# Performance work log

Measured on AMD Instinct MI355X. Metric: run time of the kernel, lower is better.

The kernel has to match this reference:

```python
import jax, jax.numpy as jnp
import numpy as np

F_, V, ED = 16, 1000, 16
B = 65536
D_IN = F_ * ED            # 256
STAR = [256, 512, 256]    # star layers
FCN = [256, 128, 64]      # mmoe expert layers
DOM, TSK, EXP = 3, 2, 8
KDT = DOM * TSK           # 6 gates/towers
SKIP_WEIGHT = 0.5
EPS = 1e-5


def layernorm(x, g, b):
    mu = jnp.mean(x, -1, keepdims=True)
    var = jnp.mean((x - mu) ** 2, -1, keepdims=True)
    return (x - mu) * jax.lax.rsqrt(var + EPS) * g + b


def mlp1(x, W, b, g, be):
    # Linear -> LayerNorm -> ReLU (MLP_N with one block)
    return jax.nn.relu(layernorm(x @ W + b, g, be))


def stack2(h, W1, b1, g1, be1, W2, b2, g2, be2):
    # vectorized bank of 2-block MLP_N experts; h: [B,D0], W1: [E,D0,D1]
    h1 = jax.nn.relu(layernorm(jnp.einsum('bd,edh->ebh', h, W1) + b1[:, None, :], g1[:, None, :], be1[:, None, :]))
    h2 = jax.nn.relu(layernorm(jnp.einsum('ebd,edh->ebh', h1, W2) + b2[:, None, :], g2[:, None, :], be2[:, None, :]))
    return h2  # [E,B,H]


def setup_inputs() -> dict:
    key = jax.random.key(0)
    ks = iter(jax.random.split(key, 64))

    def nrm(shape, scale=0.05):
        return jax.random.normal(next(ks), shape, jnp.float32) * scale

    inp = {}
    inp['x'] = jax.random.randint(next(ks), (F_, B), 0, 3).astype(jnp.int32)
    inp['emb_tables'] = nrm((F_, V, ED))
    inp['skip_W'] = nrm((D_IN, STAR[2])); inp['skip_b'] = jnp.zeros((STAR[2],))
    inp['skip_g'] = jnp.ones((STAR[2],)); inp['skip_be'] = jnp.zeros((STAR[2],))
    inp['shared_W'] = nrm((STAR[0], STAR[1])); inp['shared_b'] = jnp.zeros((STAR[1],))
    inp['slot_W'] = nrm((DOM, STAR[0], STAR[1])); inp['slot_b'] = jnp.zeros((DOM, STAR[1]))
    inp['star_W'] = nrm((STAR[1], STAR[2])); inp['star_b'] = jnp.zeros((STAR[2],))
    inp['star_g'] = jnp.ones((STAR[2],)); inp['star_be'] = jnp.zeros((STAR[2],))
    inp['dskip_W'] = nrm((KDT, STAR[2], FCN[-1])); inp['dskip_b'] = jnp.zeros((KDT, FCN[-1]))
    inp['dskip_g'] = jnp.ones((KDT, FCN[-1])); inp['dskip_be'] = jnp.zeros((KDT, FCN[-1]))
    for pre, n in (('exp', EXP), ('dexp', DOM), ('texp', TSK)):
        inp[pre + '_W1'] = nrm((n, FCN[0], FCN[1])); inp[pre + '_b1'] = jnp.zeros((n, FCN[1]))
        inp[pre + '_g1'] = jnp.ones((n, FCN[1])); inp[pre + '_be1'] = jnp.zeros((n, FCN[1]))
        inp[pre + '_W2'] = nrm((n, FCN[1], FCN[2])); inp[pre + '_b2'] = jnp.zeros((n, FCN[2]))
        inp[pre + '_g2'] = jnp.ones((n, FCN[2])); inp[pre + '_be2'] = jnp.zeros((n, FCN[2]))
    inp['gate_W'] = nrm((KDT, FCN[0], EXP)); inp['gate_b'] = jnp.zeros((KDT, EXP))
    inp['tow_W1'] = nrm((KDT, FCN[-1], FCN[-1])); inp['tow_b1'] = jnp.zeros((KDT, FCN[-1]))
    inp['tow_g'] = jnp.ones((KDT, FCN[-1])); inp['tow_be'] = jnp.zeros((KDT, FCN[-1]))
    inp['tow_W2'] = nrm((KDT, FCN[-1])); inp['tow_b2'] = jnp.zeros((KDT,))
    return inp


def _forward(x, emb_tables, skip_W, skip_b, skip_g, skip_be, shared_W, shared_b,
             slot_W, slot_b, star_W, star_b, star_g, star_be,
             dskip_W, dskip_b, dskip_g, dskip_be,
             exp_W1, exp_b1, exp_g1, exp_be1, exp_W2, exp_b2, exp_g2, exp_be2,
             dexp_W1, dexp_b1, dexp_g1, dexp_be1, dexp_W2, dexp_b2, dexp_g2, dexp_be2,
             texp_W1, texp_b1, texp_g1, texp_be1, texp_W2, texp_b2, texp_g2, texp_be2,
             gate_W, gate_b, tow_W1, tow_b1, tow_g, tow_be, tow_W2, tow_b2):
    domain_id = x[-1]                                          # [B] in {0,1,2}
    embs = jax.vmap(lambda t, i: t[i])(emb_tables, x)          # [F,B,ED]
    input_emb = jnp.moveaxis(embs, 0, 1).reshape(x.shape[1], D_IN)  # [B,256]

    skip = mlp1(input_emb, skip_W, skip_b, skip_g, skip_be)    # [B,256]

    # STAR: per-domain elementwise-product weights, domain masked select
    slot_out = jnp.einsum('bd,kdh->kbh', input_emb, slot_W * shared_W[None]) + slot_b[:, None, :] + shared_b  # [D,B,512]
    onehot = (domain_id[None, :] == jnp.arange(DOM)[:, None]).astype(slot_out.dtype)  # [D,B]
    emb0 = jnp.sum(onehot[:, :, None] * slot_out, axis=0)      # [B,512]
    emb = mlp1(emb0, star_W, star_b, star_g, star_be) + skip   # [B,256]

    # gates use emb.detach()
    gate = jax.nn.softmax(jnp.einsum('bd,kde->kbe', jax.lax.stop_gradient(emb), gate_W) + gate_b[:, None, :], axis=-1)  # [6,B,8]

    fea = stack2(emb, exp_W1, exp_b1, exp_g1, exp_be1, exp_W2, exp_b2, exp_g2, exp_be2)        # [8,B,64]
    dfea = stack2(emb, dexp_W1, dexp_b1, dexp_g1, dexp_be1, dexp_W2, dexp_b2, dexp_g2, dexp_be2)  # [3,B,64]
    tfea = stack2(emb, texp_W1, texp_b1, texp_g1, texp_be1, texp_W2, texp_b2, texp_g2, texp_be2)  # [2,B,64]
    dskip = jax.nn.relu(layernorm(jnp.einsum('bd,kdh->kbh', emb, dskip_W) + dskip_b[:, None, :], dskip_g[:, None, :], dskip_be[:, None, :]))  # [6,B,64]

    d_idx = jnp.arange(KDT) % DOM
    t_idx = jnp.arange(KDT) % TSK
    fused = jnp.einsum('kbe,ebh->kbh', gate, fea) + dfea[d_idx] + tfea[t_idx] + SKIP_WEIGHT * dskip  # [6,B,64]

    h = jax.nn.relu(layernorm(jnp.einsum('kbh,khj->kbj', fused, tow_W1) + tow_b1[:, None, :], tow_g[:, None, :], tow_be[:, None, :]))
    probs = jax.nn.sigmoid(jnp.einsum('kbh,kh->kb', h, tow_W2) + tow_b2[:, None])  # [6,B]

    # output[:, i] with i = t*DOM + d -> [B,T,D]; pick per-sample domain column
    out = jnp.moveaxis(probs, 0, 1).reshape(-1, TSK, DOM)
    result = jnp.take_along_axis(out, domain_id[:, None, None].astype(jnp.int32), axis=2)[:, :, 0]  # [B,T]
    return result


def reference(x, emb_tables, skip_W, skip_b, skip_g, skip_be, shared_W, shared_b,
              slot_W, slot_b, star_W, star_b, star_g, star_be,
              dskip_W, dskip_b, dskip_g, dskip_be,
              exp_W1, exp_b1, exp_g1, exp_be1, exp_W2, exp_b2, exp_g2, exp_be2,
              dexp_W1, dexp_b1, dexp_g1, dexp_be1, dexp_W2, dexp_b2, dexp_g2, dexp_be2,
              texp_W1, texp_b1, texp_g1, texp_be1, texp_W2, texp_b2, texp_g2, texp_be2,
              gate_W, gate_b, tow_W1, tow_b1, tow_g, tow_be, tow_W2, tow_b2):
    return _forward(x, emb_tables, skip_W, skip_b, skip_g, skip_be, shared_W, shared_b,
                    slot_W, slot_b, star_W, star_b, star_g, star_be,
                    dskip_W, dskip_b, dskip_g, dskip_be,
                    exp_W1, exp_b1, exp_g1, exp_be1, exp_W2, exp_b2, exp_g2, exp_be2,
                    dexp_W1, dexp_b1, dexp_g1, dexp_be1, dexp_W2, dexp_b2, dexp_g2, dexp_be2,
                    texp_W1, texp_b1, texp_g1, texp_be1, texp_W2, texp_b2, texp_g2, texp_be2,
                    gate_W, gate_b, tow_W1, tow_b1, tow_g, tow_be, tow_W2, tow_b2)
```

## Files before the change

### kernel.cpp

```cpp
#include <hip/hip_runtime.h>
#include <stdint.h>

#define B_TOT 65536

typedef __attribute__((ext_vector_type(8))) short s16x8;
typedef __attribute__((ext_vector_type(4))) float f32x4;
typedef unsigned short u16;
typedef unsigned int u32;

#define OFF_SKIPW   0
#define OFF_MD      65536
#define OFF_GATEW   262144
#define OFF_EXPW1   274432
#define OFF_EXPW2   700416
#define OFF_DSKIPW  806912
#define OFF_TOWW1   905216
#define OFF_BVEC    929792
#define OFF_PAR     931328
#define OFF_PARF    941568
#define OFF_EMB     944640

#define PAR_DSK  7488
#define PAR_TOW  8640
#define PAR_GB   10176
#define PAR_TB2  10224

__device__ __forceinline__ float bf2f(u16 h){ u32 v=((u32)h)<<16; return __builtin_bit_cast(float,v); }
__device__ __forceinline__ u16 f2bf(float f){
  u32 u=__builtin_bit_cast(u32,f);
  u += 0x7fffu + ((u>>16)&1u);
  return (u16)(u>>16);
}
__device__ __forceinline__ f32x4 mfma16(s16x8 a, s16x8 b, f32x4 c){
  return __builtin_amdgcn_mfma_f32_16x16x32_bf16(a,b,c,0,0,0);
}
__device__ __forceinline__ void lds_fence(){ asm volatile("s_waitcnt lgkmcnt(0)" ::: "memory"); }

__device__ __forceinline__ void gstage(const u16* gsrc, u16* ldsdst, int nbytes, int wv, int lane, int nw){
  for(int off = wv*1024; off < nbytes; off += nw*1024){
    __builtin_amdgcn_global_load_lds(
      (const __attribute__((address_space(1))) u32*)((const char*)gsrc + off + lane*16),
      (__attribute__((address_space(3))) u32*)((char*)ldsdst + off),
      16, 0, 0);
  }
}

template<int NT>
__device__ __forceinline__ void ln16(const f32x4* a, float invN, float* mu, float* rs){
  float s[4], q[4];
#pragma unroll
  for(int r=0;r<4;r++){ float aa=0.f,bb=0.f;
#pragma unroll
    for(int t=0;t<NT;t++){ float v=a[t][r]; aa+=v; bb+=v*v; }
    s[r]=aa; q[r]=bb; }
#pragma unroll
  for(int m=1;m<16;m<<=1){
#pragma unroll
    for(int r=0;r<4;r++){ s[r]+=__shfl_xor(s[r],m,16); q[r]+=__shfl_xor(q[r],m,16); } }
#pragma unroll
  for(int r=0;r<4;r++){ float m_=s[r]*invN; float v=q[r]*invN-m_*m_; mu[r]=m_; rs[r]=rsqrtf(v+1e-5f); }
}

__global__ __launch_bounds__(256) void k_pack(
    const float* __restrict__ skip_W, const float* __restrict__ gate_W,
    const float* __restrict__ exp_W1, const float* __restrict__ dexp_W1, const float* __restrict__ texp_W1,
    const float* __restrict__ exp_W2, const float* __restrict__ dexp_W2, const float* __restrict__ texp_W2,
    const float* __restrict__ dskip_W, const float* __restrict__ tow_W1,
    u16* __restrict__ ws)
{
  int i=blockIdx.x*256+threadIdx.x;
  if(i>=OFF_BVEC) return;
  if(i>=OFF_MD && i<OFF_GATEW) return;
  float v;
  if(i<OFF_MD){
    int l=i; int j=l&7, lane=(l>>3)&63, kt=(l>>9)&7, ct=l>>12;
    int n=ct*16+(lane&15), k=kt*32+((lane>>4)<<3)+j;
    v = skip_W[k*256+n];
  } else if(i<OFF_EXPW1){
    int l=i-OFF_GATEW; int j=l&7, lane=(l>>3)&63, kt=(l>>9)&7, ct=l>>12;
    int n=ct*16+(lane&15), k=kt*32+((lane>>4)<<3)+j;
    int k6=n>>3, e=n&7;
    v = gate_W[(k6*256+k)*8+e];
  } else if(i<OFF_EXPW2){
    int l=i-OFF_EXPW1; int e=l>>15, r=l&32767;
    int j=r&7, lane=(r>>3)&63, kt=(r>>9)&7, ct=r>>12;
    int n=ct*16+(lane&15), k=kt*32+((lane>>4)<<3)+j;
    v = (e<8)? exp_W1[(e*256+k)*128+n] : (e<11)? dexp_W1[((e-8)*256+k)*128+n] : texp_W1[((e-11)*256+k)*128+n];
  } else if(i<OFF_DSKIPW){
    int l=i-OFF_EXPW2; int e=l>>13, r=l&8191;
    int j=r&7, lane=(r>>3)&63, kt=(r>>9)&3, ct=r>>11;
    int n=ct*16+(lane&15), k=kt*32+((lane>>4)<<3)+j;
    v = (e<8)? exp_W2[(e*128+k)*64+n] : (e<11)? dexp_W2[((e-8)*128+k)*64+n] : texp_W2[((e-11)*128+k)*64+n];
  } else if(i<OFF_TOWW1){
    int l=i-OFF_DSKIPW; int s=l>>14, r=l&16383;
    int j=r&7, lane=(r>>3)&63, kt=(r>>9)&7, ct=r>>12;
    int n=ct*16+(lane&15), k=kt*32+((lane>>4)<<3)+j;
    v = dskip_W[(s*256+k)*64+n];
  } else {
    int l=i-OFF_TOWW1; int s=l>>12, r=l&4095;
    int j=r&7, lane=(r>>3)&63, kt=(r>>9)&1, ct=r>>10;
    int n=ct*16+(lane&15), k=kt*32+((lane>>4)<<3)+j;
    v = tow_W1[(s*64+k)*64+n];
  }
  ws[i]=f2bf(v);
}

__global__ __launch_bounds__(256) void k_packpar(
    const float* __restrict__ exp_b1,const float* __restrict__ exp_g1,const float* __restrict__ exp_be1,
    const float* __restrict__ exp_b2,const float* __restrict__ exp_g2,const float* __restrict__ exp_be2,
    const float* __restrict__ dexp_b1,const float* __restrict__ dexp_g1,const float* __restrict__ dexp_be1,
    const float* __restrict__ dexp_b2,const float* __restrict__ dexp_g2,const float* __restrict__ dexp_be2,
    const float* __restrict__ texp_b1,const float* __restrict__ texp_g1,const float* __restrict__ texp_be1,
    const float* __restrict__ texp_b2,const float* __restrict__ texp_g2,const float* __restrict__ texp_be2,
    const float* __restrict__ dskip_b,const float* __restrict__ dskip_g,const float* __restrict__ dskip_be,
    const float* __restrict__ gate_b,
    const float* __restrict__ tow_b1,const float* __restrict__ tow_g,const float* __restrict__ tow_be,
    const float* __restrict__ tow_W2,const float* __restrict__ tow_b2,
    const float* __restrict__ skip_b,const float* __restrict__ skip_g,const float* __restrict__ skip_be,
    const float* __restrict__ star_b,const float* __restrict__ star_g,const float* __restrict__ star_be,
    u16* __restrict__ ws)
{
  int i=blockIdx.x*256+threadIdx.x;
  float* parf=(float*)(ws+OFF_PARF);
  if(i<10240){
    float v=0.f;
    if(i<PAR_DSK){
      int e=i/576, r=i%576;
      const float *b1,*g1,*be1,*b2,*g2,*be2;
      if(e<8){ b1=exp_b1+e*128; g1=exp_g1+e*128; be1=exp_be1+e*128;
               b2=exp_b2+e*64;  g2=exp_g2+e*64;  be2=exp_be2+e*64; }
      else if(e<11){ int q=e-8; b1=dexp_b1+q*128; g1=dexp_g1+q*128; be1=dexp_be1+q*128;
               b2=dexp_b2+q*64; g2=dexp_g2+q*64; be2=dexp_be2+q*64; }
      else { int q=e-11; b1=texp_b1+q*128; g1=texp_g1+q*128; be1=texp_be1+q*128;
               b2=texp_b2+q*64; g2=texp_g2+q*64; be2=texp_be2+q*64; }
      v = (r<128)? b1[r] : (r<256)? g1[r-128] : (r<384)? be1[r-256]
        : (r<448)? b2[r-384] : (r<512)? g2[r-448] : be2[r-512];
    } else if(i<PAR_TOW){
      int l=i-PAR_DSK; int j=l/192, r=l%192;
      v = (r<64)? dskip_b[j*64+r] : (r<128)? dskip_g[j*64+r-64] : dskip_be[j*64+r-128];
    } else if(i<PAR_GB){
      int l=i-PAR_TOW; int k6=l/256, r=l%256;
      v = (r<64)? tow_b1[k6*64+r] : (r<128)? tow_g[k6*64+r-64]
        : (r<192)? tow_be[k6*64+r-128] : tow_W2[k6*64+r-192];
    } else if(i<PAR_TB2){ v=gate_b[i-PAR_GB]; }
    else if(i<PAR_TB2+6){ v=tow_b2[i-PAR_TB2]; }
    ws[OFF_PAR+i]=f2bf(v);
  } else if(i<10240+1536){
    int l=i-10240;
    parf[l] = (l<256)? skip_b[l] : (l<512)? skip_g[l-256] : (l<768)? skip_be[l-512]
            : (l<1024)? star_b[l-768] : (l<1280)? star_g[l-1024] : star_be[l-1280];
  }
}

__global__ __launch_bounds__(256) void k_fold(
    const float* __restrict__ slot_W, const float* __restrict__ shared_W, const float* __restrict__ star_W,
    const float* __restrict__ slot_b, const float* __restrict__ shared_b,
    u16* __restrict__ ws)
{
  __shared__ float w[512];
  int bid=blockIdx.x, tid=threadIdx.x;
  if(bid<768){
    int d=bid>>8, k=bid&255;
    for(int j=tid;j<512;j+=256) w[j]=slot_W[(d*256+k)*512+j]*shared_W[k*512+j];
    __syncthreads();
    int n=tid; float a=0.f;
    for(int j=0;j<512;j++) a += w[j]*star_W[j*256+n];
    int ct=n>>4, l15=n&15, kt=k>>5, hi=(k>>3)&3, j8=k&7;
    ws[OFF_MD + d*65536 + (((ct*8+kt)*64 + hi*16 + l15)<<3) + j8] = f2bf(a);
  } else {
    int d=bid-768;
    for(int j=tid;j<512;j+=256) w[j]=slot_b[d*512+j]+shared_b[j];
    __syncthreads();
    int n=tid; float a=0.f;
    for(int j=0;j<512;j++) a += w[j]*star_W[j*256+n];
    ((float*)(ws+OFF_BVEC))[d*256+n]=a;
  }
}

__global__ __launch_bounds__(256,2) void k_front(
    const int* __restrict__ x, const float* __restrict__ emb_tables,
    u16* __restrict__ wsu)
{
  __shared__ __align__(16) u16 shbuf[33792];
  __shared__ float bvecL[768];
  __shared__ float parF[1536];

  const int tid=threadIdx.x, lane=tid&63, wv=tid>>6;
  const int l15=lane&15, hq=lane>>4;
  const int b0=blockIdx.x*128, rowbase=b0+wv*32;
  const f32x4 fz={0.f,0.f,0.f,0.f};
  const s16x8 zf={0,0,0,0,0,0,0,0};
  u16* Wb[2]={shbuf, shbuf+8192};
  u16* trbw = shbuf + wv*8448;
  u16* embp = wsu+OFF_EMB;

  gstage(wsu+OFF_SKIPW, Wb[0], 16384, wv, lane, 4);
  gstage(wsu+OFF_BVEC, (u16*)bvecL, 3072, wv, lane, 4);
  gstage(wsu+OFF_PARF, (u16*)parF, 6144, wv, lane, 4);

  int dmA[2], dm[2][4];
#pragma unroll
  for(int rt=0;rt<2;rt++){
    dmA[rt]=x[15*B_TOT + rowbase + rt*16 + l15];
#pragma unroll
    for(int r=0;r<4;r++) dm[rt][r]=x[15*B_TOT + rowbase + rt*16 + hq*4 + r];
  }

  s16x8 af[2][8];
#pragma unroll
  for(int rt=0;rt<2;rt++){
#pragma unroll
    for(int kt=0;kt<8;kt++){
      int f=kt*2+(hq>>1), j0=(hq&1)*8;
      int row=rowbase+rt*16+l15;
      int idx=x[f*B_TOT+row];
      const float* sp=emb_tables + (size_t)(f*1000+idx)*16 + j0;
      float4 v0=*(const float4*)sp, v1=*(const float4*)(sp+4);
      union{ u16 h[8]; s16x8 v; } t;
      t.h[0]=f2bf(v0.x); t.h[1]=f2bf(v0.y); t.h[2]=f2bf(v0.z); t.h[3]=f2bf(v0.w);
      t.h[4]=f2bf(v1.x); t.h[5]=f2bf(v1.y); t.h[6]=f2bf(v1.z); t.h[7]=f2bf(v1.w);
      af[rt][kt]=t.v;
    }
  }
  __syncthreads();
  int cur=0;

  f32x4 acc[2][16];
#pragma unroll
  for(int rt=0;rt<2;rt++)
#pragma unroll
    for(int ct=0;ct<16;ct++) acc[rt][ct]=fz;

#pragma unroll
  for(int c=0;c<8;c++){
    if(c<7) gstage(wsu+OFF_SKIPW+(c+1)*8192, Wb[cur^1], 16384, wv, lane, 4);
    const u16* B=Wb[cur];
#pragma unroll
    for(int kt=0;kt<8;kt++){
#pragma unroll
      for(int i=0;i<2;i++){
        s16x8 bf=*(const s16x8*)(B + (((i*8+kt)*64+lane)<<3));
        acc[0][c*2+i]=mfma16(af[0][kt],bf,acc[0][c*2+i]);
        acc[1][c*2+i]=mfma16(af[1][kt],bf,acc[1][c*2+i]);
      }
    }
    __syncthreads(); cur^=1;
  }
#pragma unroll
  for(int rt=0;rt<2;rt++){
#pragma unroll
    for(int ct=0;ct<16;ct++){ float bb=parF[ct*16+l15];
#pragma unroll
      for(int r=0;r<4;r++) acc[rt][ct][r]+=bb; }
    float mu[4],rs[4];
    ln16<16>(&acc[rt][0], 1.f/256.f, mu, rs);
#pragma unroll
    for(int ct=0;ct<16;ct++){
      int col=ct*16+l15;
      float gv=parF[256+col], bev=parF[512+col];
#pragma unroll
      for(int r=0;r<4;r++){
        float v=fmaxf((acc[rt][ct][r]-mu[r])*rs[r]*gv+bev,0.f);
        trbw[(rt*16+hq*4+r)*264 + col]=f2bf(v);
      }
    }
  }
  lds_fence();
#pragma unroll
  for(int rt=0;rt<2;rt++){
    int rtg=(b0>>4)+wv*2+rt;
#pragma unroll
    for(int kt=0;kt<8;kt++){
      s16x8 v=*(const s16x8*)(trbw + (rt*16+l15)*264 + kt*32+hq*8);
      *(s16x8*)(embp + (((size_t)(rtg*8+kt)*64+lane)<<3)) = v;
    }
  }
  __syncthreads();
  gstage(wsu+OFF_MD, Wb[0], 16384, wv, lane, 4);
  __syncthreads();
  cur=0;

#pragma unroll
  for(int rt=0;rt<2;rt++)
#pragma unroll
    for(int ct=0;ct<16;ct++) acc[rt][ct]=fz;
  for(int d=0;d<3;d++){
#pragma unroll
    for(int c=0;c<8;c++){
      if(c<7)      gstage(wsu+OFF_MD+d*65536+(c+1)*8192, Wb[cur^1], 16384, wv, lane, 4);
      else if(d<2) gstage(wsu+OFF_MD+(d+1)*65536,        Wb[cur^1], 16384, wv, lane, 4);
      const u16* B=Wb[cur];
#pragma unroll
      for(int kt=0;kt<8;kt++){
        s16x8 a0=(dmA[0]==d)?af[0][kt]:zf;
        s16x8 a1=(dmA[1]==d)?af[1][kt]:zf;
#pragma unroll
        for(int i=0;i<2;i++){
          s16x8 bf=*(const s16x8*)(B + (((i*8+kt)*64+lane)<<3));
          acc[0][c*2+i]=mfma16(a0,bf,acc[0][c*2+i]);
          acc[1][c*2+i]=mfma16(a1,bf,acc[1][c*2+i]);
        }
      }
      __syncthreads(); cur^=1;
    }
  }

#pragma unroll
  for(int rt=0;rt<2;rt++){
#pragma unroll
    for(int ct=0;ct<16;ct++){
      int col=ct*16+l15; float sb=parF[768+col];
#pragma unroll
      for(int r=0;r<4;r++) acc[rt][ct][r] += sb + bvecL[dm[rt][r]*256+col];
    }
    float mu[4],rs[4];
    ln16<16>(&acc[rt][0], 1.f/256.f, mu, rs);
#pragma unroll
    for(int ct=0;ct<16;ct++){
      int col=ct*16+l15;
      float gv=parF[1024+col], bev=parF[1280+col];
#pragma unroll
      for(int r=0;r<4;r++){
        float v=fmaxf((acc[rt][ct][r]-mu[r])*rs[r]*gv+bev,0.f);
        trbw[(rt*16+hq*4+r)*264 + col]=f2bf(v);
      }
    }
  }
  lds_fence();
#pragma unroll
  for(int rt=0;rt<2;rt++){
    int rtg=(b0>>4)+wv*2+rt;
#pragma unroll
    for(int kt=0;kt<8;kt++){
      s16x8 vs=*(const s16x8*)(trbw + (rt*16+l15)*264 + kt*32+hq*8);
      s16x8 vk=*(const s16x8*)(embp + (((size_t)(rtg*8+kt)*64+lane)<<3));
      union{ u16 h[8]; s16x8 v; } t;
#pragma unroll
      for(int j=0;j<8;j++) t.h[j]=f2bf(bf2f((u16)vs[j])+bf2f((u16)vk[j]));
      *(s16x8*)(embp + (((size_t)(rtg*8+kt)*64+lane)<<3)) = t.v;
    }
  }
}

__device__ __forceinline__ int phase_off(int p){
  if(p<2)  return OFF_GATEW + p*8192;
  if(p<67){ int q=p-2, u=q/5, s=q%5;
            return (s<4)? (OFF_EXPW1+u*32768+s*8192) : (OFF_EXPW2+u*8192); }
  if(p<79){ int q=p-67; return OFF_DSKIPW + (q>>1)*16384 + (q&1)*8192; }
  return OFF_TOWW1 + (p-79)*8192;
}
__device__ __forceinline__ void stage16k(const u16* g, u16* l, int wv, int lane){
  __builtin_amdgcn_global_load_lds(
    (const __attribute__((address_space(1))) u32*)((const char*)g + wv*1024 + lane*16),
    (__attribute__((address_space(3))) u32*)((char*)l + wv*1024), 16,0,0);
  __builtin_amdgcn_global_load_lds(
    (const __attribute__((address_space(1))) u32*)((const char*)g + 8192 + wv*1024 + lane*16),
    (__attribute__((address_space(3))) u32*)((char*)l + 8192 + wv*1024), 16,0,0);
}
__device__ __forceinline__ void endph2(){ asm volatile("s_waitcnt vmcnt(2)\n\ts_barrier" ::: "memory"); }
__device__ __forceinline__ void endph0(){ asm volatile("s_waitcnt vmcnt(0)\n\ts_barrier" ::: "memory"); }

__global__ __launch_bounds__(512,2) void k_B(
    const int* __restrict__ x, u16* __restrict__ wsu, float* __restrict__ out)
{
  __shared__ __align__(16) u16 Wb[3][8192];
  __shared__ __align__(16) u16 trb[8][32][136];
  __shared__ __align__(16) u16 parAll[10240];
  __shared__ __align__(16) u32 gateF[256][8];

  const int tid=threadIdx.x, lane=tid&63, wv=tid>>6;
  const int l15=lane&15, hq=lane>>4;
  const int b0=blockIdx.x*256, rowbase=b0+wv*32;
  const f32x4 fz={0.f,0.f,0.f,0.f};
  const u16* embp=wsu+OFF_EMB;
  u16* trbw=&trb[wv][0][0];

  gstage(wsu+OFF_PAR, parAll, 20480, wv, lane, 8);
  stage16k(wsu+phase_off(0), &Wb[0][0], wv, lane);
  stage16k(wsu+phase_off(1), &Wb[1][0], wv, lane);

  int dm[2][4];
#pragma unroll
  for(int rt=0;rt<2;rt++)
#pragma unroll
    for(int r=0;r<4;r++) dm[rt][r]=x[15*B_TOT + rowbase + rt*16 + hq*4 + r];

  s16x8 af[2][8];
#pragma unroll
  for(int rt=0;rt<2;rt++){
    int rtg=(rowbase>>4)+rt;
#pragma unroll
    for(int kt=0;kt<8;kt++)
      af[rt][kt]=*(const s16x8*)(embp + (((size_t)(rtg*8+kt)*64+lane)<<3));
  }

  f32x4 fa0[2][4], fa1[2][4];
#pragma unroll
  for(int rt=0;rt<2;rt++)
#pragma unroll
    for(int ct=0;ct<4;ct++){ fa0[rt][ct]=fz; fa1[rt][ct]=fz; }

  __syncthreads();
  int p=0;

  {
    f32x4 gacc[2][3];
#pragma unroll
    for(int rt=0;rt<2;rt++)
#pragma unroll
      for(int ct=0;ct<3;ct++) gacc[rt][ct]=fz;
    stage16k(wsu+phase_off(2), &Wb[2][0], wv, lane);
#pragma unroll
    for(int kt=0;kt<8;kt++)
#pragma unroll
      for(int i=0;i<2;i++){
        s16x8 bf=*(const s16x8*)(&Wb[0][0] + (((i*8+kt)*64+lane)<<3));
        gacc[0][i]=mfma16(af[0][kt],bf,gacc[0][i]);
        gacc[1][i]=mfma16(af[1][kt],bf,gacc[1][i]);
      }
    endph2(); p=1;

    stage16k(wsu+phase_off(3), &Wb[0][0], wv, lane);
#pragma unroll
    for(int kt=0;kt<8;kt++){
      s16x8 bf=*(const s16x8*)(&Wb[1][0] + ((kt*64+lane)<<3));
      gacc[0][2]=mfma16(af[0][kt],bf,gacc[0][2]);
      gacc[1][2]=mfma16(af[1][kt],bf,gacc[1][2]);
    }
    u16* gFh=(u16*)&gateF[0][0];
#pragma unroll
    for(int rt=0;rt<2;rt++)
#pragma unroll
      for(int ct=0;ct<3;ct++){
        int k6=ct*2+(l15>>3), e=l15&7;
        float gb=bf2f(parAll[PAR_GB + k6*8+e]);
#pragma unroll
        for(int r=0;r<4;r++){
          float v=gacc[rt][ct][r]+gb;
          float mx=v;
          mx=fmaxf(mx,__shfl_xor(mx,1,8)); mx=fmaxf(mx,__shfl_xor(mx,2,8)); mx=fmaxf(mx,__shfl_xor(mx,4,8));
          float pe=__expf(v-mx);
          float ss=pe;
          ss+=__shfl_xor(ss,1,8); ss+=__shfl_xor(ss,2,8); ss+=__shfl_xor(ss,4,8);
          int brow=wv*32+rt*16+hq*4+r;
          int dmv=dm[rt][r];
          if(k6==dmv)   gFh[(brow*8+e)*2]  =f2bf(pe/ss);
          if(k6==3+dmv) gFh[(brow*8+e)*2+1]=f2bf(pe/ss);
        }
      }
    lds_fence();
    endph2(); p=2;
  }

  for(int u=0;u<13;u++){
    f32x4 acc1[2][8];
#pragma unroll
    for(int rt=0;rt<2;rt++)
#pragma unroll
      for(int ct=0;ct<8;ct++) acc1[rt][ct]=fz;
    for(int c=0;c<4;c++){
      const u16* Bw=&Wb[p%3][0];
      stage16k(wsu+phase_off(p+2), &Wb[(p+2)%3][0], wv, lane);
#pragma unroll
      for(int kt=0;kt<8;kt++)
#pragma unroll
        for(int i=0;i<2;i++){
          s16x8 bf=*(const s16x8*)(Bw + (((i*8+kt)*64+lane)<<3));
          acc1[0][c*2+i]=mfma16(af[0][kt],bf,acc1[0][c*2+i]);
          acc1[1][c*2+i]=mfma16(af[1][kt],bf,acc1[1][c*2+i]);
        }
      endph2(); p++;
    }
    {
      const u16* Bw=&Wb[p%3][0];
      stage16k(wsu+phase_off(p+2), &Wb[(p+2)%3][0], wv, lane);
      const int pb=u*576;
#pragma unroll
      for(int rt=0;rt<2;rt++){
#pragma unroll
        for(int ct=0;ct<8;ct++){ float bb=bf2f(parAll[pb+ct*16+l15]);
#pragma unroll
          for(int r=0;r<4;r++) acc1[rt][ct][r]+=bb; }
        float mu[4],rs[4],nm[4];
        ln16<8>(&acc1[rt][0],1.f/128.f,mu,rs);
#pragma unroll
        for(int r=0;r<4;r++) nm[r]=-mu[r]*rs[r];
#pragma unroll
        for(int ct=0;ct<8;ct++){
          int col=ct*16+l15;
          float gv=bf2f(parAll[pb+128+col]), bev=bf2f(parAll[pb+256+col]);
#pragma unroll
          for(int r=0;r<4;r++){
            float vn=fmaf(acc1[rt][ct][r],rs[r],nm[r]);
            trbw[(rt*16+hq*4+r)*136+col]=f2bf(fmaxf(fmaf(vn,gv,bev),0.f));
          }
        }
      }
      lds_fence();
      s16x8 af2[2][4];
#pragma unroll
      for(int rt=0;rt<2;rt++)
#pragma unroll
        for(int kt=0;kt<4;kt++)
          af2[rt][kt]=*(const s16x8*)(trbw+(rt*16+l15)*136+kt*32+hq*8);
      f32x4 acc2[2][4];
#pragma unroll
      for(int rt=0;rt<2;rt++)
#pragma unroll
        for(int ct=0;ct<4;ct++) acc2[rt][ct]=fz;
#pragma unroll
      for(int kt=0;kt<4;kt++)
#pragma unroll
        for(int ct=0;ct<4;ct++){
          s16x8 bf=*(const s16x8*)(Bw + (((ct*4+kt)*64+lane)<<3));
          acc2[0][ct]=mfma16(af2[0][kt],bf,acc2[0][ct]);
          acc2[1][ct]=mfma16(af2[1][kt],bf,acc2[1][ct]);
        }
#pragma unroll
      for(int rt=0;rt<2;rt++){
#pragma unroll
        for(int ct=0;ct<4;ct++){ float bb=bf2f(parAll[pb+384+ct*16+l15]);
#pragma unroll
          for(int r=0;r<4;r++) acc2[rt][ct][r]+=bb; }
        float mu[4],rs[4],nm[4];
        ln16<4>(&acc2[rt][0],1.f/64.f,mu,rs);
#pragma unroll
        for(int r=0;r<4;r++) nm[r]=-mu[r]*rs[r];
        float g0v[4],g1v[4];
        if(u<8){
#pragma unroll
          for(int r=0;r<4;r++){ u32 gg=gateF[wv*32+rt*16+hq*4+r][u];
            g0v[r]=bf2f((u16)(gg&0xffffu)); g1v[r]=bf2f((u16)(gg>>16)); }
        } else if(u<11){
#pragma unroll
          for(int r=0;r<4;r++){ float m=(dm[rt][r]==u-8)?1.f:0.f; g0v[r]=m; g1v[r]=m; }
        } else {
          int q=u-11;
#pragma unroll
          for(int r=0;r<4;r++){
            g0v[r]=((dm[rt][r]&1)==q)?1.f:0.f;
            g1v[r]=(((dm[rt][r]+1)&1)==q)?1.f:0.f;
          }
        }
#pragma unroll
        for(int ct=0;ct<4;ct++){
          int col=ct*16+l15;
          float gv=bf2f(parAll[pb+448+col]), bev=bf2f(parAll[pb+512+col]);
#pragma unroll
          for(int r=0;r<4;r++){
            float vn=fmaf(acc2[rt][ct][r],rs[r],nm[r]);
            float o=fmaxf(fmaf(vn,gv,bev),0.f);
            fa0[rt][ct][r]=fmaf(g0v[r],o,fa0[rt][ct][r]);
            fa1[rt][ct][r]=fmaf(g1v[r],o,fa1[rt][ct][r]);
          }
        }
      }
      endph2(); p++;
    }
  }

  for(int j=0;j<6;j++){
    f32x4 a3[2][4];
#pragma unroll
    for(int rt=0;rt<2;rt++)
#pragma unroll
      for(int ct=0;ct<4;ct++) a3[rt][ct]=fz;
    for(int c=0;c<2;c++){
      const u16* Bw=&Wb[p%3][0];
      if(p+2<82) stage16k(wsu+phase_off(p+2), &Wb[(p+2)%3][0], wv, lane);
#pragma unroll
      for(int kt=0;kt<8;kt++)
#pragma unroll
        for(int i=0;i<2;i++){
          s16x8 bf=*(const s16x8*)(Bw + (((i*8+kt)*64+lane)<<3));
          a3[0][c*2+i]=mfma16(af[0][kt],bf,a3[0][c*2+i]);
          a3[1][c*2+i]=mfma16(af[1][kt],bf,a3[1][c*2+i]);
        }
      if(c==1){
        const int pb=PAR_DSK+j*192, dj=j%3;
#pragma unroll
        for(int rt=0;rt<2;rt++){
#pragma unroll
          for(int ct=0;ct<4;ct++){ float bb=bf2f(parAll[pb+ct*16+l15]);
#pragma unroll
            for(int r=0;r<4;r++) a3[rt][ct][r]+=bb; }
          float mu[4],rs[4],nm[4],mk[4];
          ln16<4>(&a3[rt][0],1.f/64.f,mu,rs);
#pragma unroll
          for(int r=0;r<4;r++){ nm[r]=-mu[r]*rs[r]; mk[r]=(dm[rt][r]==dj)?0.5f:0.f; }
#pragma unroll
          for(int ct=0;ct<4;ct++){
            int col=ct*16+l15;
            float gv=bf2f(parAll[pb+64+col]), bev=bf2f(parAll[pb+128+col]);
#pragma unroll
            for(int r=0;r<4;r++){
              float vn=fmaf(a3[rt][ct][r],rs[r],nm[r]);
              float o=fmaxf(fmaf(vn,gv,bev),0.f);
              if(j<3) fa0[rt][ct][r]=fmaf(mk[r],o,fa0[rt][ct][r]);
              else    fa1[rt][ct][r]=fmaf(mk[r],o,fa1[rt][ct][r]);
            }
          }
        }
      }
      endph2(); p++;
    }
  }

#pragma unroll
  for(int rt=0;rt<2;rt++)
#pragma unroll
    for(int ct=0;ct<4;ct++)
#pragma unroll
      for(int r=0;r<4;r++){
        int rr=(rt*16+hq*4+r)*136 + ct*16+l15;
        trbw[rr]   =f2bf(fa0[rt][ct][r]);
        trbw[rr+64]=f2bf(fa1[rt][ct][r]);
      }
  lds_fence();
  s16x8 aft0[2][2], aft1[2][2];
#pragma unroll
  for(int rt=0;rt<2;rt++)
#pragma unroll
    for(int kt=0;kt<2;kt++){
      aft0[rt][kt]=*(const s16x8*)(trbw+(rt*16+l15)*136+kt*32+hq*8);
      aft1[rt][kt]=*(const s16x8*)(trbw+(rt*16+l15)*136+64+kt*32+hq*8);
    }

  for(int ph=0;ph<3;ph++){
    const u16* Bw=&Wb[p%3][0];
    if(p+2<82) stage16k(wsu+phase_off(p+2), &Wb[(p+2)%3][0], wv, lane);
#pragma unroll
    for(int s=0;s<2;s++){
      int k6=ph*2+s;
      int T0=(k6<3);
      int d=T0?k6:(k6-3);
      f32x4 ta[2][4];
#pragma unroll
      for(int rt=0;rt<2;rt++)
#pragma unroll
        for(int ct=0;ct<4;ct++) ta[rt][ct]=fz;
#pragma unroll
      for(int kt=0;kt<2;kt++)
#pragma unroll
        for(int ct=0;ct<4;ct++){
          s16x8 bf=*(const s16x8*)(Bw + s*4096 + (((ct*2+kt)*64+lane)<<3));
          if(T0){ ta[0][ct]=mfma16(aft0[0][kt],bf,ta[0][ct]); ta[1][ct]=mfma16(aft0[1][kt],bf,ta[1][ct]); }
          else  { ta[0][ct]=mfma16(aft1[0][kt],bf,ta[0][ct]); ta[1][ct]=mfma16(aft1[1][kt],bf,ta[1][ct]); }
        }
      const int pb=PAR_TOW+k6*256;
#pragma unroll
      for(int rt=0;rt<2;rt++){
#pragma unroll
        for(int ct=0;ct<4;ct++){ float bb=bf2f(parAll[pb+ct*16+l15]);
#pragma unroll
          for(int r=0;r<4;r++) ta[rt][ct][r]+=bb; }
        float mu[4],rs[4],nm[4];
        ln16<4>(&ta[rt][0],1.f/64.f,mu,rs);
#pragma unroll
        for(int r=0;r<4;r++) nm[r]=-mu[r]*rs[r];
        float pr[4]={0.f,0.f,0.f,0.f};
#pragma unroll
        for(int ct=0;ct<4;ct++){
          int col=ct*16+l15;
          float gv=bf2f(parAll[pb+64+col]), bev=bf2f(parAll[pb+128+col]), w2=bf2f(parAll[pb+192+col]);
#pragma unroll
          for(int r=0;r<4;r++){
            float vn=fmaf(ta[rt][ct][r],rs[r],nm[r]);
            float o=fmaxf(fmaf(vn,gv,bev),0.f);
            pr[r]=fmaf(o,w2,pr[r]);
          }
        }
#pragma unroll
        for(int m=1;m<16;m<<=1){
#pragma unroll
          for(int r=0;r<4;r++) pr[r]+=__shfl_xor(pr[r],m,16);
        }
        if(l15==0){
          float tb2=bf2f(parAll[PAR_TB2+k6]);
#pragma unroll
          for(int r=0;r<4;r++){
            if(dm[rt][r]==d){
              float sv=pr[r]+tb2;
              out[(size_t)(rowbase+rt*16+hq*4+r)*2 + (T0?0:1)] = 1.f/(1.f+__expf(-sv));
            }
          }
        }
      }
    }
    if(ph==0) endph2(); else if(ph==1) endph0();
    p++;
  }
}

extern "C" void kernel_launch(void* const* d_in, const int* in_sizes, int n_in,
                              void* d_out, int out_size, void* d_ws, size_t ws_size,
                              hipStream_t stream)
{
  const int*   x          =(const int*)  d_in[0];
  const float* emb_tables =(const float*)d_in[1];
  const float* skip_W     =(const float*)d_in[2];
  const float* skip_b     =(const float*)d_in[3];
  const float* skip_g     =(const float*)d_in[4];
  const float* skip_be    =(const float*)d_in[5];
  const float* shared_W   =(const float*)d_in[6];
  const float* shared_b   =(const float*)d_in[7];
  const float* slot_W     =(const float*)d_in[8];
  const float* slot_b     =(const float*)d_in[9];
  const float* star_W     =(const float*)d_in[10];
  const float* star_b     =(const float*)d_in[11];
  const float* star_g     =(const float*)d_in[12];
  const float* star_be    =(const float*)d_in[13];
  const float* dskip_W    =(const float*)d_in[14];
  const float* dskip_b    =(const float*)d_in[15];
  const float* dskip_g    =(const float*)d_in[16];
  const float* dskip_be   =(const float*)d_in[17];
  const float* exp_W1     =(const float*)d_in[18];
  const float* exp_b1     =(const float*)d_in[19];
  const float* exp_g1     =(const float*)d_in[20];
  const float* exp_be1    =(const float*)d_in[21];
  const float* exp_W2     =(const float*)d_in[22];
  const float* exp_b2     =(const float*)d_in[23];
  const float* exp_g2     =(const float*)d_in[24];
  const float* exp_be2    =(const float*)d_in[25];
  const float* dexp_W1    =(const float*)d_in[26];
  const float* dexp_b1    =(const float*)d_in[27];
  const float* dexp_g1    =(const float*)d_in[28];
  const float* dexp_be1   =(const float*)d_in[29];
  const float* dexp_W2    =(const float*)d_in[30];
  const float* dexp_b2    =(const float*)d_in[31];
  const float* dexp_g2    =(const float*)d_in[32];
  const float* dexp_be2   =(const float*)d_in[33];
  const float* texp_W1    =(const float*)d_in[34];
  const float* texp_b1    =(const float*)d_in[35];
  const float* texp_g1    =(const float*)d_in[36];
  const float* texp_be1   =(const float*)d_in[37];
  const float* texp_W2    =(const float*)d_in[38];
  const float* texp_b2    =(const float*)d_in[39];
  const float* texp_g2    =(const float*)d_in[40];
  const float* texp_be2   =(const float*)d_in[41];
  const float* gate_W     =(const float*)d_in[42];
  const float* gate_b     =(const float*)d_in[43];
  const float* tow_W1     =(const float*)d_in[44];
  const float* tow_b1     =(const float*)d_in[45];
  const float* tow_g      =(const float*)d_in[46];
  const float* tow_be     =(const float*)d_in[47];
  const float* tow_W2     =(const float*)d_in[48];
  const float* tow_b2     =(const float*)d_in[49];

  u16* wsu=(u16*)d_ws;
  float* out=(float*)d_out;

  k_pack<<<(OFF_BVEC+255)/256,256,0,stream>>>(skip_W,gate_W,
      exp_W1,dexp_W1,texp_W1,exp_W2,dexp_W2,texp_W2,dskip_W,tow_W1,wsu);
  k_packpar<<<46,256,0,stream>>>(
      exp_b1,exp_g1,exp_be1,exp_b2,exp_g2,exp_be2,
      dexp_b1,dexp_g1,dexp_be1,dexp_b2,dexp_g2,dexp_be2,
      texp_b1,texp_g1,texp_be1,texp_b2,texp_g2,texp_be2,
      dskip_b,dskip_g,dskip_be,gate_b,
      tow_b1,tow_g,tow_be,tow_W2,tow_b2,
      skip_b,skip_g,skip_be,star_b,star_g,star_be,wsu);
  k_fold<<<771,256,0,stream>>>(slot_W,shared_W,star_W,slot_b,shared_b,wsu);
  k_front<<<B_TOT/128,256,0,stream>>>(x,emb_tables,wsu);
  k_B<<<B_TOT/256,512,0,stream>>>(x,wsu,out);
}
```

Baseline: 383.7 us.

## Sort rows by domain so blocks run only their domain's weights

Adds count and scatter kernels that build a domain-sorted permutation of batch rows, with each domain padded to a multiple of 256. The front and main kernels then process rows in permuted order. Each block handles a single domain and stages and multiplies only that domain's star, expert, skip and tower weights instead of all three with masking. The cost is three extra small launches, global atomics, gathered (less coalesced) row loads and output writes, and up to 512 padded rows of wasted work.

```diff
diff --git a/kernel.cpp b/kernel.cpp
--- a/kernel.cpp
+++ b/kernel.cpp
@@ -2,11 +2,13 @@
 #include <stdint.h>
 
 #define B_TOT 65536
+#define B_PAD 66048
 
 typedef __attribute__((ext_vector_type(8))) short s16x8;
 typedef __attribute__((ext_vector_type(4))) float f32x4;
 typedef unsigned short u16;
 typedef unsigned int u32;
+typedef unsigned long long u64;
 
 #define OFF_SKIPW   0
 #define OFF_MD      65536
@@ -19,6 +21,8 @@
 #define OFF_PAR     931328
 #define OFF_PARF    941568
 #define OFF_EMB     944640
+#define OFF_PERM    17852928
+#define OFF_CNT     17985024
 
 #define PAR_DSK  7488
 #define PAR_TOW  8640
@@ -59,6 +63,48 @@
     for(int r=0;r<4;r++){ s[r]+=__shfl_xor(s[r],m,16); q[r]+=__shfl_xor(q[r],m,16); } }
 #pragma unroll
   for(int r=0;r<4;r++){ float m_=s[r]*invN; float v=q[r]*invN-m_*m_; mu[r]=m_; rs[r]=rsqrtf(v+1e-5f); }
+}
+
+__global__ __launch_bounds__(256) void k_sortinit(u16* __restrict__ ws){
+  int i=blockIdx.x*256+threadIdx.x;
+  u32* perm=(u32*)(ws+OFF_PERM);
+  if(i<B_PAD) perm[i]=0x80000000u;
+  if(i<8) ((u32*)(ws+OFF_CNT))[i]=0u;
+}
+__global__ __launch_bounds__(256) void k_count(const int* __restrict__ x, u16* __restrict__ ws){
+  u32* cnt=(u32*)(ws+OFF_CNT);
+  int i=blockIdx.x*256+threadIdx.x;
+  int lane=threadIdx.x&63;
+  int d=x[15*B_TOT+i];
+  u64 m0=__ballot(d==0), m1=__ballot(d==1), m2=__ballot(d==2);
+  if(lane==0){
+    if(m0) atomicAdd(&cnt[0],(u32)__popcll(m0));
+    if(m1) atomicAdd(&cnt[1],(u32)__popcll(m1));
+    if(m2) atomicAdd(&cnt[2],(u32)__popcll(m2));
+  }
+}
+__global__ __launch_bounds__(256) void k_scatter(const int* __restrict__ x, u16* __restrict__ ws){
+  u32* cnt=(u32*)(ws+OFF_CNT);
+  u32* perm=(u32*)(ws+OFF_PERM);
+  int i=blockIdx.x*256+threadIdx.x;
+  int lane=threadIdx.x&63;
+  int d=x[15*B_TOT+i];
+  u32 c0=cnt[0], c1=cnt[1];
+  u32 s1=(c0+255u)&~255u, s2=s1+((c1+255u)&~255u);
+  u64 m0=__ballot(d==0), m1=__ballot(d==1), m2=__ballot(d==2);
+  u32 b0v=0,b1v=0,b2v=0;
+  if(lane==0){
+    if(m0) b0v=atomicAdd(&cnt[3],(u32)__popcll(m0));
+    if(m1) b1v=atomicAdd(&cnt[4],(u32)__popcll(m1));
+    if(m2) b2v=atomicAdd(&cnt[5],(u32)__popcll(m2));
+  }
+  b0v=__shfl(b0v,0,64); b1v=__shfl(b1v,0,64); b2v=__shfl(b2v,0,64);
+  u64 below=(1ull<<lane)-1ull;
+  u32 pos;
+  if(d==0)      pos=      b0v+(u32)__popcll(m0&below);
+  else if(d==1) pos=s1+   b1v+(u32)__popcll(m1&below);
+  else          pos=s2+   b2v+(u32)__popcll(m2&below);
+  perm[pos]=(u32)i;
 }
 
 __global__ __launch_bounds__(256) void k_pack(
@@ -182,38 +228,31 @@
     u16* __restrict__ wsu)
 {
   __shared__ __align__(16) u16 shbuf[33792];
-  __shared__ float bvecL[768];
+  __shared__ float bvecL[256];
   __shared__ float parF[1536];
 
   const int tid=threadIdx.x, lane=tid&63, wv=tid>>6;
   const int l15=lane&15, hq=lane>>4;
   const int b0=blockIdx.x*128, rowbase=b0+wv*32;
   const f32x4 fz={0.f,0.f,0.f,0.f};
-  const s16x8 zf={0,0,0,0,0,0,0,0};
   u16* Wb[2]={shbuf, shbuf+8192};
   u16* trbw = shbuf + wv*8448;
   u16* embp = wsu+OFF_EMB;
+  const u32* perm=(const u32*)(wsu+OFF_PERM);
 
   gstage(wsu+OFF_SKIPW, Wb[0], 16384, wv, lane, 4);
-  gstage(wsu+OFF_BVEC, (u16*)bvecL, 3072, wv, lane, 4);
+  const int d = x[15*B_TOT + (int)(perm[b0]&0x7fffffffu)];
+  gstage(wsu+OFF_BVEC + d*512, (u16*)bvecL, 1024, wv, lane, 4);
   gstage(wsu+OFF_PARF, (u16*)parF, 6144, wv, lane, 4);
 
-  int dmA[2], dm[2][4];
+  s16x8 af[2][8];
 #pragma unroll
   for(int rt=0;rt<2;rt++){
-    dmA[rt]=x[15*B_TOT + rowbase + rt*16 + l15];
-#pragma unroll
-    for(int r=0;r<4;r++) dm[rt][r]=x[15*B_TOT + rowbase + rt*16 + hq*4 + r];
-  }
-
-  s16x8 af[2][8];
-#pragma unroll
-  for(int rt=0;rt<2;rt++){
+    int prow=(int)(perm[rowbase+rt*16+l15]&0x7fffffffu);
 #pragma unroll
     for(int kt=0;kt<8;kt++){
       int f=kt*2+(hq>>1), j0=(hq&1)*8;
-      int row=rowbase+rt*16+l15;
-      int idx=x[f*B_TOT+row];
+      int idx=x[f*B_TOT+prow];
       const float* sp=emb_tables + (size_t)(f*1000+idx)*16 + j0;
       float4 v0=*(const float4*)sp, v1=*(const float4*)(sp+4);
       union{ u16 h[8]; s16x8 v; } t;
@@ -276,7 +315,7 @@
     }
   }
   __syncthreads();
-  gstage(wsu+OFF_MD, Wb[0], 16384, wv, lane, 4);
+  gstage(wsu+OFF_MD+d*65536, Wb[0], 16384, wv, lane, 4);
   __syncthreads();
   cur=0;
 
@@ -284,25 +323,20 @@
   for(int rt=0;rt<2;rt++)
 #pragma unroll
     for(int ct=0;ct<16;ct++) acc[rt][ct]=fz;
-  for(int d=0;d<3;d++){
-#pragma unroll
-    for(int c=0;c<8;c++){
-      if(c<7)      gstage(wsu+OFF_MD+d*65536+(c+1)*8192, Wb[cur^1], 16384, wv, lane, 4);
-      else if(d<2) gstage(wsu+OFF_MD+(d+1)*65536,        Wb[cur^1], 16384, wv, lane, 4);
-      const u16* B=Wb[cur];
-#pragma unroll
-      for(int kt=0;kt<8;kt++){
-        s16x8 a0=(dmA[0]==d)?af[0][kt]:zf;
-        s16x8 a1=(dmA[1]==d)?af[1][kt]:zf;
-#pragma unroll
-        for(int i=0;i<2;i++){
-          s16x8 bf=*(const s16x8*)(B + (((i*8+kt)*64+lane)<<3));
-          acc[0][c*2+i]=mfma16(a0,bf,acc[0][c*2+i]);
-          acc[1][c*2+i]=mfma16(a1,bf,acc[1][c*2+i]);
-        }
-      }
-      __syncthreads(); cur^=1;
-    }
+#pragma unroll
+  for(int c=0;c<8;c++){
+    if(c<7) gstage(wsu+OFF_MD+d*65536+(c+1)*8192, Wb[cur^1], 16384, wv, lane, 4);
+    const u16* B=Wb[cur];
+#pragma unroll
+    for(int kt=0;kt<8;kt++){
+#pragma unroll
+      for(int i=0;i<2;i++){
+        s16x8 bf=*(const s16x8*)(B + (((i*8+kt)*64+lane)<<3));
+        acc[0][c*2+i]=mfma16(af[0][kt],bf,acc[0][c*2+i]);
+        acc[1][c*2+i]=mfma16(af[1][kt],bf,acc[1][c*2+i]);
+      }
+    }
+    __syncthreads(); cur^=1;
   }
 
 #pragma unroll
@@ -311,7 +345,7 @@
     for(int ct=0;ct<16;ct++){
       int col=ct*16+l15; float sb=parF[768+col];
 #pragma unroll
-      for(int r=0;r<4;r++) acc[rt][ct][r] += sb + bvecL[dm[rt][r]*256+col];
+      for(int r=0;r<4;r++) acc[rt][ct][r] += sb + bvecL[col];
     }
     float mu[4],rs[4];
     ln16<16>(&acc[rt][0], 1.f/256.f, mu, rs);
@@ -342,20 +376,31 @@
   }
 }
 
-__device__ __forceinline__ int phase_off(int p){
-  if(p<2)  return OFF_GATEW + p*8192;
-  if(p<67){ int q=p-2, u=q/5, s=q%5;
+__device__ __forceinline__ int phase_src(int p, int d){
+  if(p<2) return OFF_GATEW + p*8192;
+  if(p<57){ int q=p-2, ui=q/5, s=q%5;
+            int u = (ui<8)? ui : (ui==8)? (8+d) : (11+(ui-9));
             return (s<4)? (OFF_EXPW1+u*32768+s*8192) : (OFF_EXPW2+u*8192); }
-  if(p<79){ int q=p-67; return OFF_DSKIPW + (q>>1)*16384 + (q&1)*8192; }
-  return OFF_TOWW1 + (p-79)*8192;
-}
-__device__ __forceinline__ void stage16k(const u16* g, u16* l, int wv, int lane){
+  if(p<61){ int q=p-57; int j=(q>>1)? (3+d) : d;
+            return OFF_DSKIPW + j*16384 + (q&1)*8192; }
+  return -1;
+}
+__device__ __forceinline__ void stage8k(const u16* g, u16* l, int wv, int lane){
   __builtin_amdgcn_global_load_lds(
     (const __attribute__((address_space(1))) u32*)((const char*)g + wv*1024 + lane*16),
     (__attribute__((address_space(3))) u32*)((char*)l + wv*1024), 16,0,0);
-  __builtin_amdgcn_global_load_lds(
-    (const __attribute__((address_space(1))) u32*)((const char*)g + 8192 + wv*1024 + lane*16),
-    (__attribute__((address_space(3))) u32*)((char*)l + 8192 + wv*1024), 16,0,0);
+}
+__device__ __forceinline__ void stage16k(const u16* g, u16* l, int wv, int lane){
+  stage8k(g,      l,      wv, lane);
+  stage8k(g+4096, l+4096, wv, lane);
+}
+__device__ __forceinline__ void stage_phase(int p, int d, const u16* wsu, u16* slot, int wv, int lane){
+  if(p==61){
+    stage8k(wsu+OFF_TOWW1+d*4096,     slot,      wv, lane);
+    stage8k(wsu+OFF_TOWW1+(3+d)*4096, slot+4096, wv, lane);
+  } else {
+    stage16k(wsu+phase_src(p,d), slot, wv, lane);
+  }
 }
 __device__ __forceinline__ void endph2(){ asm volatile("s_waitcnt vmcnt(2)\n\ts_barrier" ::: "memory"); }
 __device__ __forceinline__ void endph0(){ asm volatile("s_waitcnt vmcnt(0)\n\ts_barrier" ::: "memory"); }
@@ -373,17 +418,20 @@
   const int b0=blockIdx.x*256, rowbase=b0+wv*32;
   const f32x4 fz={0.f,0.f,0.f,0.f};
   const u16* embp=wsu+OFF_EMB;
+  const u32* perm=(const u32*)(wsu+OFF_PERM);
   u16* trbw=&trb[wv][0][0];
 
   gstage(wsu+OFF_PAR, parAll, 20480, wv, lane, 8);
-  stage16k(wsu+phase_off(0), &Wb[0][0], wv, lane);
-  stage16k(wsu+phase_off(1), &Wb[1][0], wv, lane);
-
-  int dm[2][4];
+  stage16k(wsu+OFF_GATEW,      &Wb[0][0], wv, lane);
+  stage16k(wsu+OFF_GATEW+8192, &Wb[1][0], wv, lane);
+
+  const int d = x[15*B_TOT + (int)(perm[b0]&0x7fffffffu)];
+
+  u32 pv[2][4];
 #pragma unroll
   for(int rt=0;rt<2;rt++)
 #pragma unroll
-    for(int r=0;r<4;r++) dm[rt][r]=x[15*B_TOT + rowbase + rt*16 + hq*4 + r];
+    for(int r=0;r<4;r++) pv[rt][r]=perm[rowbase + rt*16 + hq*4 + r];
 
   s16x8 af[2][8];
 #pragma unroll
@@ -409,7 +457,7 @@
     for(int rt=0;rt<2;rt++)
 #pragma unroll
       for(int ct=0;ct<3;ct++) gacc[rt][ct]=fz;
-    stage16k(wsu+phase_off(2), &Wb[2][0], wv, lane);
+    stage_phase(2, d, wsu, &Wb[2][0], wv, lane);
 #pragma unroll
     for(int kt=0;kt<8;kt++)
 #pragma unroll
@@ -420,7 +468,7 @@
       }
     endph2(); p=1;
 
-    stage16k(wsu+phase_off(3), &Wb[0][0], wv, lane);
+    stage_phase(3, d, wsu, &Wb[0][0], wv, lane);
 #pragma unroll
     for(int kt=0;kt<8;kt++){
       s16x8 bf=*(const s16x8*)(&Wb[1][0] + ((kt*64+lane)<<3));
@@ -443,16 +491,16 @@
           float ss=pe;
           ss+=__shfl_xor(ss,1,8); ss+=__shfl_xor(ss,2,8); ss+=__shfl_xor(ss,4,8);
           int brow=wv*32+rt*16+hq*4+r;
-          int dmv=dm[rt][r];
-          if(k6==dmv)   gFh[(brow*8+e)*2]  =f2bf(pe/ss);
-          if(k6==3+dmv) gFh[(brow*8+e)*2+1]=f2bf(pe/ss);
+          if(k6==d)   gFh[(brow*8+e)*2]  =f2bf(pe/ss);
+          if(k6==3+d) gFh[(brow*8+e)*2+1]=f2bf(pe/ss);
         }
       }
     lds_fence();
     endph2(); p=2;
   }
 
-  for(int u=0;u<13;u++){
+  for(int ui=0;ui<11;ui++){
+    const int u = (ui<8)? ui : (ui==8)? (8+d) : (11+(ui-9));
     f32x4 acc1[2][8];
 #pragma unroll
     for(int rt=0;rt<2;rt++)
@@ -460,7 +508,7 @@
       for(int ct=0;ct<8;ct++) acc1[rt][ct]=fz;
     for(int c=0;c<4;c++){
       const u16* Bw=&Wb[p%3][0];
-      stage16k(wsu+phase_off(p+2), &Wb[(p+2)%3][0], wv, lane);
+      stage_phase(p+2, d, wsu, &Wb[(p+2)%3][0], wv, lane);
 #pragma unroll
       for(int kt=0;kt<8;kt++)
 #pragma unroll
@@ -473,7 +521,7 @@
     }
     {
       const u16* Bw=&Wb[p%3][0];
-      stage16k(wsu+phase_off(p+2), &Wb[(p+2)%3][0], wv, lane);
+      stage_phase(p+2, d, wsu, &Wb[(p+2)%3][0], wv, lane);
       const int pb=u*576;
 #pragma unroll
       for(int rt=0;rt<2;rt++){
@@ -516,6 +564,9 @@
           acc2[0][ct]=mfma16(af2[0][kt],bf,acc2[0][ct]);
           acc2[1][ct]=mfma16(af2[1][kt],bf,acc2[1][ct]);
         }
+      float g0u=1.f, g1u=1.f;
+      if(ui==9){  g0u=((d&1)==0)?1.f:0.f; g1u=(((d+1)&1)==0)?1.f:0.f; }
+      if(ui==10){ g0u=((d&1)==1)?1.f:0.f; g1u=(((d+1)&1)==1)?1.f:0.f; }
 #pragma unroll
       for(int rt=0;rt<2;rt++){
 #pragma unroll
@@ -527,20 +578,13 @@
 #pragma unroll
         for(int r=0;r<4;r++) nm[r]=-mu[r]*rs[r];
         float g0v[4],g1v[4];
-        if(u<8){
-#pragma unroll
-          for(int r=0;r<4;r++){ u32 gg=gateF[wv*32+rt*16+hq*4+r][u];
+        if(ui<8){
+#pragma unroll
+          for(int r=0;r<4;r++){ u32 gg=gateF[wv*32+rt*16+hq*4+r][ui];
             g0v[r]=bf2f((u16)(gg&0xffffu)); g1v[r]=bf2f((u16)(gg>>16)); }
-        } else if(u<11){
-#pragma unroll
-          for(int r=0;r<4;r++){ float m=(dm[rt][r]==u-8)?1.f:0.f; g0v[r]=m; g1v[r]=m; }
         } else {
-          int q=u-11;
-#pragma unroll
-          for(int r=0;r<4;r++){
-            g0v[r]=((dm[rt][r]&1)==q)?1.f:0.f;
-            g1v[r]=(((dm[rt][r]+1)&1)==q)?1.f:0.f;
-          }
+#pragma unroll
+          for(int r=0;r<4;r++){ g0v[r]=g0u; g1v[r]=g1u; }
         }
 #pragma unroll
         for(int ct=0;ct<4;ct++){
@@ -559,7 +603,8 @@
     }
   }
 
-  for(int j=0;j<6;j++){
+  for(int ji=0;ji<2;ji++){
+    const int jj = ji? (3+d) : d;
     f32x4 a3[2][4];
 #pragma unroll
     for(int rt=0;rt<2;rt++)
@@ -567,7 +612,7 @@
       for(int ct=0;ct<4;ct++) a3[rt][ct]=fz;
     for(int c=0;c<2;c++){
       const u16* Bw=&Wb[p%3][0];
-      if(p+2<82) stage16k(wsu+phase_off(p+2), &Wb[(p+2)%3][0], wv, lane);
+      if(p+2<=61) stage_phase(p+2, d, wsu, &Wb[(p+2)%3][0], wv, lane);
 #pragma unroll
       for(int kt=0;kt<8;kt++)
 #pragma unroll
@@ -577,17 +622,17 @@
           a3[1][c*2+i]=mfma16(af[1][kt],bf,a3[1][c*2+i]);
         }
       if(c==1){
-        const int pb=PAR_DSK+j*192, dj=j%3;
+        const int pb=PAR_DSK+jj*192;
 #pragma unroll
         for(int rt=0;rt<2;rt++){
 #pragma unroll
           for(int ct=0;ct<4;ct++){ float bb=bf2f(parAll[pb+ct*16+l15]);
 #pragma unroll
             for(int r=0;r<4;r++) a3[rt][ct][r]+=bb; }
-          float mu[4],rs[4],nm[4],mk[4];
+          float mu[4],rs[4],nm[4];
           ln16<4>(&a3[rt][0],1.f/64.f,mu,rs);
 #pragma unroll
-          for(int r=0;r<4;r++){ nm[r]=-mu[r]*rs[r]; mk[r]=(dm[rt][r]==dj)?0.5f:0.f; }
+          for(int r=0;r<4;r++) nm[r]=-mu[r]*rs[r];
 #pragma unroll
           for(int ct=0;ct<4;ct++){
             int col=ct*16+l15;
@@ -596,13 +641,14 @@
             for(int r=0;r<4;r++){
               float vn=fmaf(a3[rt][ct][r],rs[r],nm[r]);
               float o=fmaxf(fmaf(vn,gv,bev),0.f);
-              if(j<3) fa0[rt][ct][r]=fmaf(mk[r],o,fa0[rt][ct][r]);
-              else    fa1[rt][ct][r]=fmaf(mk[r],o,fa1[rt][ct][r]);
+              if(ji==0) fa0[rt][ct][r]=fmaf(0.5f,o,fa0[rt][ct][r]);
+              else      fa1[rt][ct][r]=fmaf(0.5f,o,fa1[rt][ct][r]);
             }
           }
         }
       }
-      endph2(); p++;
+      if(ji==1 && c==1) endph0(); else endph2();
+      p++;
     }
   }
 
@@ -626,14 +672,11 @@
       aft1[rt][kt]=*(const s16x8*)(trbw+(rt*16+l15)*136+64+kt*32+hq*8);
     }
 
-  for(int ph=0;ph<3;ph++){
+  {
     const u16* Bw=&Wb[p%3][0];
-    if(p+2<82) stage16k(wsu+phase_off(p+2), &Wb[(p+2)%3][0], wv, lane);
 #pragma unroll
     for(int s=0;s<2;s++){
-      int k6=ph*2+s;
-      int T0=(k6<3);
-      int d=T0?k6:(k6-3);
+      const int k6 = s? (3+d) : d;
       f32x4 ta[2][4];
 #pragma unroll
       for(int rt=0;rt<2;rt++)
@@ -644,8 +687,8 @@
 #pragma unroll
         for(int ct=0;ct<4;ct++){
           s16x8 bf=*(const s16x8*)(Bw + s*4096 + (((ct*2+kt)*64+lane)<<3));
-          if(T0){ ta[0][ct]=mfma16(aft0[0][kt],bf,ta[0][ct]); ta[1][ct]=mfma16(aft0[1][kt],bf,ta[1][ct]); }
-          else  { ta[0][ct]=mfma16(aft1[0][kt],bf,ta[0][ct]); ta[1][ct]=mfma16(aft1[1][kt],bf,ta[1][ct]); }
+          if(s==0){ ta[0][ct]=mfma16(aft0[0][kt],bf,ta[0][ct]); ta[1][ct]=mfma16(aft0[1][kt],bf,ta[1][ct]); }
+          else    { ta[0][ct]=mfma16(aft1[0][kt],bf,ta[0][ct]); ta[1][ct]=mfma16(aft1[1][kt],bf,ta[1][ct]); }
         }
       const int pb=PAR_TOW+k6*256;
 #pragma unroll
@@ -679,16 +722,15 @@
           float tb2=bf2f(parAll[PAR_TB2+k6]);
 #pragma unroll
           for(int r=0;r<4;r++){
-            if(dm[rt][r]==d){
+            u32 pvv=pv[rt][r];
+            if(!(pvv>>31)){
               float sv=pr[r]+tb2;
-              out[(size_t)(rowbase+rt*16+hq*4+r)*2 + (T0?0:1)] = 1.f/(1.f+__expf(-sv));
+              out[(size_t)pvv*2 + s] = 1.f/(1.f+__expf(-sv));
             }
           }
         }
       }
     }
-    if(ph==0) endph2(); else if(ph==1) endph0();
-    p++;
   }
 }
 
@@ -696,6 +738,8 @@
                               void* d_out, int out_size, void* d_ws, size_t ws_size,
                               hipStream_t stream)
 {
+  if(ws_size < (size_t)(OFF_CNT+32)*2) return;
+
   const int*   x          =(const int*)  d_in[0];
   const float* emb_tables =(const float*)d_in[1];
   const float* skip_W     =(const float*)d_in[2];
@@ -750,6 +794,9 @@
   u16* wsu=(u16*)d_ws;
   float* out=(float*)d_out;
 
+  k_sortinit<<<B_PAD/256,256,0,stream>>>(wsu);
+  k_count<<<B_TOT/256,256,0,stream>>>(x,wsu);
+  k_scatter<<<B_TOT/256,256,0,stream>>>(x,wsu);
   k_pack<<<(OFF_BVEC+255)/256,256,0,stream>>>(skip_W,gate_W,
       exp_W1,dexp_W1,texp_W1,exp_W2,dexp_W2,texp_W2,dskip_W,tow_W1,wsu);
   k_packpar<<<46,256,0,stream>>>(
@@ -760,6 +807,6 @@
       tow_b1,tow_g,tow_be,tow_W2,tow_b2,
       skip_b,skip_g,skip_be,star_b,star_g,star_be,wsu);
   k_fold<<<771,256,0,stream>>>(slot_W,shared_W,star_W,slot_b,shared_b,wsu);
-  k_front<<<B_TOT/128,256,0,stream>>>(x,emb_tables,wsu);
-  k_B<<<B_TOT/256,512,0,stream>>>(x,wsu,out);
-}
+  k_front<<<B_PAD/128,256,0,stream>>>(x,emb_tables,wsu);
+  k_B<<<B_PAD/256,512,0,stream>>>(x,wsu,out);
+}
```

Result: slower. 543.1 us (+41.5%).
